# Kernel tuning notes

Hardware: AMD Instinct MI355X
Metric: run time of the kernel (lower is better)

Reference implementation:

```python
import jax, jax.numpy as jnp
import numpy as np

B_, L_ = 32, 4096
D_MODEL, D_STATE, D_CONV, EXPAND, N_LAYERS, HORIZON = 128, 16, 4, 2, 4, 1
D_INNER = EXPAND * D_MODEL
DT_RANK = (D_MODEL + 15) // 16  # ceil(d_model/16) = 8
EPS = 1e-6


def setup_inputs() -> dict:
    key = jax.random.key(0)
    ks = jax.random.split(key, 10)
    s = lambda k, sh, sc: jax.random.normal(k, sh, jnp.float32) * sc
    inp = {}
    inp["x"] = s(ks[0], (B_, L_, 1), 1.0)
    inp["input_proj_w"] = s(ks[1], (D_MODEL, 1), 0.5)
    inp["input_proj_b"] = jnp.zeros((D_MODEL,), jnp.float32)
    inp["in_proj_w"] = s(ks[2], (N_LAYERS, 2 * D_INNER, D_MODEL), D_MODEL ** -0.5)
    inp["conv_w"] = s(ks[3], (N_LAYERS, D_INNER, 1, D_CONV), D_CONV ** -0.5)
    inp["conv_b"] = jnp.zeros((N_LAYERS, D_INNER), jnp.float32)
    inp["x_proj_w"] = s(ks[4], (N_LAYERS, DT_RANK + 2 * D_STATE, D_INNER), D_INNER ** -0.5)
    inp["dt_proj_w"] = s(ks[5], (N_LAYERS, D_INNER, DT_RANK), DT_RANK ** -0.5)
    inp["dt_proj_b"] = jnp.full((N_LAYERS, D_INNER), -4.0, jnp.float32)
    inp["A_log"] = jnp.tile(jnp.log(jnp.arange(1, D_STATE + 1, dtype=jnp.float32))[None, None, :], (N_LAYERS, D_INNER, 1))
    inp["D"] = jnp.ones((N_LAYERS, D_INNER), jnp.float32)
    inp["out_proj_w"] = s(ks[6], (N_LAYERS, D_MODEL, D_INNER), D_INNER ** -0.5)
    inp["norm_w"] = jnp.ones((D_MODEL,), jnp.float32)
    inp["output_proj_w"] = s(ks[7], (HORIZON, D_MODEL), D_MODEL ** -0.5)
    inp["output_proj_b"] = jnp.zeros((HORIZON,), jnp.float32)
    return inp


def _mamba_block(h, in_w, cw, cb, xpw, dtw, dtb, alog, d_skip, ow):
    # h: [B, L, d_model] -> [B, L, d_model]
    xz = jnp.einsum('bld,ed->ble', h, in_w)            # [B, L, 2*d_inner]
    x, z = jnp.split(xz, 2, axis=-1)                   # each [B, L, d_inner]
    # depthwise causal conv over time
    xc = jax.lax.conv_general_dilated(
        x.transpose(0, 2, 1), cw, window_strides=(1,),
        padding=[(D_CONV - 1, 0)], feature_group_count=D_INNER,
        dimension_numbers=('NCH', 'OIH', 'NCH'))      # [B, d_inner, L]
    x = jax.nn.silu(xc.transpose(0, 2, 1) + cb)        # [B, L, d_inner]
    dbl = jnp.einsum('blc,ec->ble', x, xpw)            # [B, L, dt_rank+2*d_state]
    dt, Bm, Cm = jnp.split(dbl, [DT_RANK, DT_RANK + D_STATE], axis=-1)
    dt = jax.nn.softplus(jnp.einsum('blr,cr->blc', dt, dtw) + dtb)  # [B, L, d_inner]
    A = -jnp.exp(alog)                                  # [d_inner, d_state]

    def step(hst, inputs):
        dt_t, B_t, C_t, x_t = inputs                   # [B,c],[B,s],[B,s],[B,c]
        hst = jnp.exp(dt_t[..., None] * A) * hst + (dt_t * x_t)[..., None] * B_t[:, None, :]
        y = jnp.einsum('bcs,bs->bc', hst, C_t)
        return hst, y

    h0 = jnp.zeros((x.shape[0], D_INNER, D_STATE), x.dtype)
    xs = (dt.transpose(1, 0, 2), Bm.transpose(1, 0, 2), Cm.transpose(1, 0, 2), x.transpose(1, 0, 2))
    _, ys = jax.lax.scan(step, h0, xs)                 # [L, B, d_inner]
    y = ys.transpose(1, 0, 2) + d_skip * x             # skip: y += D * x
    y = y * jax.nn.silu(z)                             # gating
    return jnp.einsum('blc,dc->bld', y, ow)            # [B, L, d_model]


def reference(x, input_proj_w, input_proj_b, in_proj_w, conv_w, conv_b, x_proj_w,
              dt_proj_w, dt_proj_b, A_log, D, out_proj_w, norm_w,
              output_proj_w, output_proj_b):
    h = jnp.einsum('blo,do->bld', x, input_proj_w) + input_proj_b  # [B, L, d_model]
    for i in range(N_LAYERS):
        h = h + _mamba_block(h, in_proj_w[i], conv_w[i], conv_b[i], x_proj_w[i],
                             dt_proj_w[i], dt_proj_b[i], A_log[i], D[i], out_proj_w[i])
    rms = jnp.sqrt(jnp.mean(h * h, axis=-1, keepdims=True) + EPS)
    h = norm_w * h / rms
    return h[:, -1, :] @ output_proj_w.T + output_proj_b  # [B, horizon]
```

## Files before the change

### kernel.cpp

```cpp
#include <hip/hip_runtime.h>

#define B_    32
#define L_    4096
#define DM    128
#define DI    256
#define DS_   16
#define RANK  8
#define NL    4
#define M_    (B_*L_)
#define NC    64
#define CL    (L_/NC)

typedef __attribute__((ext_vector_type(8))) short short8;
typedef __attribute__((ext_vector_type(4))) float floatx4;
typedef __attribute__((ext_vector_type(2))) float float2v;

__device__ __forceinline__ float b2f(unsigned short u) {
    return __uint_as_float(((unsigned)u) << 16);
}
__device__ __forceinline__ unsigned short f2b(float f) {
    unsigned u = __float_as_uint(f);
    unsigned r = u + 0x7fffu + ((u >> 16) & 1u);
    return (unsigned short)(r >> 16);
}
__device__ __forceinline__ float fast_sig(float v) {
    return __builtin_amdgcn_rcpf(1.f + __expf(-v));
}

__global__ __launch_bounds__(256) void k_detect(const unsigned short* __restrict__ x,
                                                int* __restrict__ flag) {
    __shared__ int cnt;
    if (threadIdx.x == 0) cnt = 0;
    __syncthreads();
    int ok = 0;
    for (int i = 0; i < 4; ++i) {
        unsigned short u = x[threadIdx.x * 4 + i];
        int e = (u >> 7) & 0xFF;
        if ((u & 0x7FFF) == 0 || (e >= 100 && e <= 150)) ok++;
    }
    atomicAdd(&cnt, ok);
    __syncthreads();
    if (threadIdx.x == 0) *flag = (cnt >= 800) ? 1 : 0;
}

struct CvtSeg { const void* src; float* dst; int n; };
struct CvtPack { CvtSeg seg[11]; };
__global__ __launch_bounds__(256) void k_cvt_params(CvtPack p, const int* __restrict__ flag) {
    int s = blockIdx.y;
    int i = blockIdx.x * 256 + threadIdx.x;
    if (i >= p.seg[s].n) return;
    p.seg[s].dst[i] = (*flag) ? b2f(((const unsigned short*)p.seg[s].src)[i])
                              : ((const float*)p.seg[s].src)[i];
}
__global__ __launch_bounds__(256) void k_cvt16(const void* __restrict__ src,
                                               unsigned short* __restrict__ dst,
                                               int n, const int* __restrict__ flag) {
    int i = blockIdx.x * 256 + threadIdx.x;
    if (i >= n) return;
    if (*flag) dst[i] = ((const unsigned short*)src)[i];
    else       dst[i] = f2b(((const float*)src)[i]);
}
__global__ __launch_bounds__(256) void k_xpw48(const void* __restrict__ src,
                                               unsigned short* __restrict__ dst,
                                               const int* __restrict__ flag) {
    int i = blockIdx.x * 256 + threadIdx.x;
    int col = i & 255, rowl = (i >> 8) % 48, layer = i / (48*256);
    unsigned short v = 0;
    if (rowl < 40) {
        int si = (layer*40 + rowl)*256 + col;
        v = (*flag) ? ((const unsigned short*)src)[si] : f2b(((const float*)src)[si]);
    }
    dst[i] = v;
}

__global__ __launch_bounds__(256) void k_init(const void* __restrict__ xraw,
                                              const int* __restrict__ flag,
                                              const float* __restrict__ ipw,
                                              const float* __restrict__ ipb,
                                              float* __restrict__ h, int base) {
    int idx = blockIdx.x * 256 + threadIdx.x;
    int bl = idx >> 7, d = idx & 127;
    float x = (*flag) ? b2f(((const unsigned short*)xraw)[base + bl])
                      : ((const float*)xraw)[base + bl];
    h[idx] = x * ipw[d] + ipb[d];
}

__global__ __launch_bounds__(256) void k_gemm_in(const float* __restrict__ h,
                                                 const unsigned short* __restrict__ w,
                                                 unsigned short* __restrict__ xb,
                                                 unsigned short* __restrict__ zb) {
    __shared__ unsigned short lA[64][136];
    __shared__ unsigned short lW[256][40];
    int tid = threadIdx.x;
    int lane = tid & 63, wv = tid >> 6;
    int ln = lane & 15, qd = lane >> 4;
    int r0 = blockIdx.x * 64;
    int n0 = blockIdx.y * 256;

    {
        int r = tid >> 2;
        int c0 = (tid & 3) * 32;
        const float4* src = (const float4*)(h + (size_t)(r0 + r) * DM + c0);
        for (int j = 0; j < 8; ++j) {
            float4 v = src[j];
            lA[r][c0 + j*4 + 0] = f2b(v.x);
            lA[r][c0 + j*4 + 1] = f2b(v.y);
            lA[r][c0 + j*4 + 2] = f2b(v.z);
            lA[r][c0 + j*4 + 3] = f2b(v.w);
        }
    }

    floatx4 acc[16];
    for (int i = 0; i < 16; ++i) acc[i] = (floatx4)0.f;

    for (int kc = 0; kc < 4; ++kc) {
        __syncthreads();
        {
            int n = tid;
            const uint4* src = (const uint4*)(w + (size_t)(n0 + n) * DM + kc * 32);
            uint4 a = src[0], b = src[1], c = src[2], d = src[3];
            *(uint4*)&lW[n][0]  = a;
            *(uint4*)&lW[n][8]  = b;
            *(uint4*)&lW[n][16] = c;
            *(uint4*)&lW[n][24] = d;
        }
        __syncthreads();
        short8 af = *(const short8*)&lA[wv*16 + ln][kc*32 + qd*8];
        for (int nt = 0; nt < 16; ++nt) {
            short8 bf = *(const short8*)&lW[nt*16 + ln][qd*8];
            acc[nt] = __builtin_amdgcn_mfma_f32_16x16x32_bf16(af, bf, acc[nt], 0, 0, 0);
        }
    }

    for (int nt = 0; nt < 16; ++nt)
        for (int rg = 0; rg < 4; ++rg) {
            size_t gr = (size_t)(r0 + wv*16 + qd*4 + rg);
            int gc = nt*16 + ln;
            unsigned short v = f2b(acc[nt][rg]);
            if (blockIdx.y == 0) xb[gr*DI + gc] = v;
            else                 zb[gr*DI + gc] = v;
        }
}

__device__ __forceinline__ bool a_is_integer_ladder(const float* A) {
    bool f = true;
    #pragma unroll
    for (int s = 0; s < DS_; ++s)
        f = f && (fabsf(A[s] + (float)(s+1)) < 0.01f * (float)(s+1));
    return f;
}

__device__ __forceinline__ void unpack8(uint4 p, float* f) {
    f[0] = b2f((unsigned short)(p.x & 0xffff)); f[1] = b2f((unsigned short)(p.x >> 16));
    f[2] = b2f((unsigned short)(p.y & 0xffff)); f[3] = b2f((unsigned short)(p.y >> 16));
    f[4] = b2f((unsigned short)(p.z & 0xffff)); f[5] = b2f((unsigned short)(p.z >> 16));
    f[6] = b2f((unsigned short)(p.w & 0xffff)); f[7] = b2f((unsigned short)(p.w >> 16));
}

__global__ __launch_bounds__(256) void k_xprojc(const unsigned short* __restrict__ xb,
                                                const float* __restrict__ cw,
                                                const float* __restrict__ cbp,
                                                const unsigned short* __restrict__ w48,
                                                const float* __restrict__ dtw,
                                                const float* __restrict__ dtb,
                                                const float* __restrict__ alog,
                                                unsigned short* __restrict__ xcg,
                                                unsigned short* __restrict__ dtg,
                                                unsigned short* __restrict__ Bg,
                                                unsigned short* __restrict__ Cg,
                                                float* __restrict__ Pbuf,
                                                float* __restrict__ Hbuf) {
    __shared__ unsigned short lA[64][264];
    __shared__ unsigned short lW[48][40];
    __shared__ float ldbl[64][8];
    __shared__ float lBs[64][DS_];
    int tid = threadIdx.x;
    int lane = tid & 63, wv = tid >> 6;
    int ln = lane & 15, qd = lane >> 4;
    int r0 = blockIdx.x * 64;
    int l0 = r0 & (L_ - 1);
    int bidx = r0 >> 12;
    int kidx = l0 >> 6;

    {
        int c = tid;
        float w0 = cw[c*4+0], w1 = cw[c*4+1], w2 = cw[c*4+2], w3 = cw[c*4+3];
        float bias = cbp[c];
        float x0 = (l0 >= 3) ? b2f(xb[(size_t)(r0-3)*DI + c]) : 0.f;
        float x1 = (l0 >= 2) ? b2f(xb[(size_t)(r0-2)*DI + c]) : 0.f;
        float x2 = (l0 >= 1) ? b2f(xb[(size_t)(r0-1)*DI + c]) : 0.f;
        for (int r = 0; r < 64; ++r) {
            float xcur = b2f(xb[(size_t)(r0+r)*DI + c]);
            float v = w0*x0 + w1*x1 + w2*x2 + w3*xcur + bias;
            float s = v * fast_sig(v);
            unsigned short sb = f2b(s);
            lA[r][c] = sb;
            xcg[(size_t)(r0+r)*DI + c] = sb;
            x0 = x1; x1 = x2; x2 = xcur;
        }
    }

    floatx4 acc[3];
    for (int i = 0; i < 3; ++i) acc[i] = (floatx4)0.f;

    for (int kc = 0; kc < 8; ++kc) {
        __syncthreads();
        if (tid < 192) {
            int n = tid >> 2, q = tid & 3;
            *(uint4*)&lW[n][q*8] = *(const uint4*)(w48 + (size_t)n*DI + kc*32 + q*8);
        }
        __syncthreads();
        short8 af = *(const short8*)&lA[wv*16 + ln][kc*32 + qd*8];
        for (int nt = 0; nt < 3; ++nt) {
            short8 bf = *(const short8*)&lW[nt*16 + ln][qd*8];
            acc[nt] = __builtin_amdgcn_mfma_f32_16x16x32_bf16(af, bf, acc[nt], 0, 0, 0);
        }
    }

    for (int nt = 0; nt < 3; ++nt)
        for (int rg = 0; rg < 4; ++rg) {
            int rloc = wv*16 + qd*4 + rg;
            size_t row = (size_t)(r0 + rloc);
            int n = nt*16 + ln;
            float v = acc[nt][rg];
            if (n < 8)       ldbl[rloc][n] = v;
            else if (n < 24) {
                unsigned short bv = f2b(v);
                Bg[row*DS_ + (n-8)] = bv;
                lBs[rloc][n-8] = b2f(bv);
            }
            else if (n < 40) Cg[row*DS_ + (n-24)] = f2b(v);
        }
    __syncthreads();

    {
        int c = tid;
        float w8[8];
        #pragma unroll
        for (int j = 0; j < 8; ++j) w8[j] = dtw[c*8 + j];
        float bias = dtb[c];
        float A[DS_];
        #pragma unroll
        for (int j = 0; j < 4; ++j) {
            float4 a4 = *(const float4*)(alog + c*DS_ + j*4);
            A[j*4+0] = -__expf(a4.x); A[j*4+1] = -__expf(a4.y);
            A[j*4+2] = -__expf(a4.z); A[j*4+3] = -__expf(a4.w);
        }
        float P[DS_];
        if (a_is_integer_ladder(A)) {
            float2v h2[8];
            #pragma unroll
            for (int j = 0; j < 8; ++j) h2[j] = (float2v)0.f;
            float S = 0.f;
            for (int r = 0; r < 64; ++r) {
                float a = bias;
                #pragma unroll
                for (int j = 0; j < 8; ++j) a += ldbl[r][j] * w8[j];
                float sp = (a > 20.f) ? a : __logf(1.f + __expf(a));
                unsigned short spb = f2b(sp);
                dtg[(size_t)(r0+r)*DI + c] = spb;
                float dtv = b2f(spb);
                float du = dtv * b2f(lA[r][c]);
                float Bl[DS_];
                *(float4*)&Bl[0]  = *(const float4*)&lBs[r][0];
                *(float4*)&Bl[4]  = *(const float4*)&lBs[r][4];
                *(float4*)&Bl[8]  = *(const float4*)&lBs[r][8];
                *(float4*)&Bl[12] = *(const float4*)&lBs[r][12];
                float E = __expf(-dtv);
                float E2 = E * E;
                float2v ep[8];
                ep[0].x = E; ep[0].y = E2;
                float2v E22; E22.x = E2; E22.y = E2;
                #pragma unroll
                for (int j = 1; j < 8; ++j) ep[j] = ep[j-1] * E22;
                float2v du2; du2.x = du; du2.y = du;
                #pragma unroll
                for (int j = 0; j < 8; ++j) {
                    float2v bj; bj.x = Bl[2*j]; bj.y = Bl[2*j+1];
                    h2[j] = ep[j]*h2[j] + du2*bj;
                }
                S += dtv;
            }
            #pragma unroll
            for (int s = 0; s < DS_; ++s) P[s] = __expf(-(float)(s+1) * S);
            float4* pp = (float4*)(Pbuf + (((size_t)bidx*NC + kidx)*DI + c)*DS_);
            float4* ph = (float4*)(Hbuf + (((size_t)bidx*NC + kidx)*DI + c)*DS_);
            #pragma unroll
            for (int j = 0; j < 4; ++j) {
                pp[j] = make_float4(P[j*4+0], P[j*4+1], P[j*4+2], P[j*4+3]);
                ph[j] = make_float4(h2[j*2].x, h2[j*2].y, h2[j*2+1].x, h2[j*2+1].y);
            }
        } else {
            float h[DS_];
            #pragma unroll
            for (int s = 0; s < DS_; ++s) { h[s] = 0.f; P[s] = 1.f; }
            for (int r = 0; r < 64; ++r) {
                float a = bias;
                #pragma unroll
                for (int j = 0; j < 8; ++j) a += ldbl[r][j] * w8[j];
                float sp = (a > 20.f) ? a : __logf(1.f + __expf(a));
                unsigned short spb = f2b(sp);
                dtg[(size_t)(r0+r)*DI + c] = spb;
                float dtv = b2f(spb);
                float du = dtv * b2f(lA[r][c]);
                float Bl[DS_];
                *(float4*)&Bl[0]  = *(const float4*)&lBs[r][0];
                *(float4*)&Bl[4]  = *(const float4*)&lBs[r][4];
                *(float4*)&Bl[8]  = *(const float4*)&lBs[r][8];
                *(float4*)&Bl[12] = *(const float4*)&lBs[r][12];
                #pragma unroll
                for (int s = 0; s < DS_; ++s) {
                    float e = __expf(dtv * A[s]);
                    h[s] = e*h[s] + du*Bl[s];
                    P[s] *= e;
                }
            }
            float4* pp = (float4*)(Pbuf + (((size_t)bidx*NC + kidx)*DI + c)*DS_);
            float4* ph = (float4*)(Hbuf + (((size_t)bidx*NC + kidx)*DI + c)*DS_);
            #pragma unroll
            for (int j = 0; j < 4; ++j) {
                pp[j] = make_float4(P[j*4+0], P[j*4+1], P[j*4+2], P[j*4+3]);
                ph[j] = make_float4(h[j*4+0], h[j*4+1], h[j*4+2], h[j*4+3]);
            }
        }
    }
}

__global__ __launch_bounds__(256) void k_scan2(const float* __restrict__ Pbuf,
                                               float* __restrict__ Hbuf,
                                               int cb) {
    int t = blockIdx.x * 256 + threadIdx.x;
    if (t >= cb * DI * DS_) return;
    int b  = t / (DI * DS_);
    int cs = t % (DI * DS_);
    float H = 0.f;
    for (int k = 0; k < NC; ++k) {
        size_t idx = ((size_t)b * NC + k) * (DI * DS_) + cs;
        float P  = Pbuf[idx];
        float he = Hbuf[idx];
        Hbuf[idx] = H;
        H = P * H + he;
    }
}

__global__ __launch_bounds__(256) void k_scan3g(const unsigned short* __restrict__ dtg,
                                                const unsigned short* __restrict__ xcg,
                                                const unsigned short* __restrict__ Bg,
                                                const unsigned short* __restrict__ Cg,
                                                const float* __restrict__ alog,
                                                const float* __restrict__ Hbuf,
                                                const unsigned short* __restrict__ zb,
                                                const float* __restrict__ Dp,
                                                unsigned short* __restrict__ yg) {
    __shared__ float lB[CL*DS_];
    __shared__ float lC[CL*DS_];
    int c = threadIdx.x;
    int k = blockIdx.x, b = blockIdx.y;
    size_t row0 = (size_t)b * L_ + (size_t)k * CL;
    {
        int t = c & 127;
        const unsigned short* src = (c < 128) ? (Bg + row0*DS_) : (Cg + row0*DS_);
        float* dst = (c < 128) ? lB : lC;
        uint4 p = ((const uint4*)src)[t];
        float f[8]; unpack8(p, f);
        *(float4*)&dst[t*8]     = make_float4(f[0], f[1], f[2], f[3]);
        *(float4*)&dst[t*8 + 4] = make_float4(f[4], f[5], f[6], f[7]);
    }
    float A[DS_];
    #pragma unroll
    for (int j = 0; j < 4; ++j) {
        float4 a4 = *(const float4*)(alog + c*DS_ + j*4);
        A[j*4+0] = -__expf(a4.x); A[j*4+1] = -__expf(a4.y);
        A[j*4+2] = -__expf(a4.z); A[j*4+3] = -__expf(a4.w);
    }
    float Dc = Dp[c];
    __syncthreads();
    const unsigned short* pdt = dtg + row0*DI + c;
    const unsigned short* pxc = xcg + row0*DI + c;
    const unsigned short* pz  = zb  + row0*DI + c;
    unsigned short* py        = yg  + row0*DI + c;
    float dtc = b2f(*pdt), xcc = b2f(*pxc), zc = b2f(*pz);

    if (a_is_integer_ladder(A)) {
        float2v h2[8];
        {
            const float4* ph = (const float4*)(Hbuf + (((size_t)b*NC + k)*DI + c)*DS_);
            #pragma unroll
            for (int j = 0; j < 4; ++j) {
                float4 v = ph[j];
                h2[j*2].x = v.x; h2[j*2].y = v.y;
                h2[j*2+1].x = v.z; h2[j*2+1].y = v.w;
            }
        }
        for (int l = 0; l < CL; ++l) {
            float dtn = b2f(pdt[DI]); float xcn = b2f(pxc[DI]); float zn = b2f(pz[DI]);
            float du = dtc * xcc;
            float Bl[DS_], Cl[DS_];
            *(float4*)&Bl[0]  = *(const float4*)&lB[l*DS_ + 0];
            *(float4*)&Bl[4]  = *(const float4*)&lB[l*DS_ + 4];
            *(float4*)&Bl[8]  = *(const float4*)&lB[l*DS_ + 8];
            *(float4*)&Bl[12] = *(const float4*)&lB[l*DS_ + 12];
            *(float4*)&Cl[0]  = *(const float4*)&lC[l*DS_ + 0];
            *(float4*)&Cl[4]  = *(const float4*)&lC[l*DS_ + 4];
            *(float4*)&Cl[8]  = *(const float4*)&lC[l*DS_ + 8];
            *(float4*)&Cl[12] = *(const float4*)&lC[l*DS_ + 12];
            float E = __expf(-dtc);
            float E2 = E * E;
            float2v ep[8];
            ep[0].x = E; ep[0].y = E2;
            float2v E22; E22.x = E2; E22.y = E2;
            #pragma unroll
            for (int j = 1; j < 8; ++j) ep[j] = ep[j-1] * E22;
            float2v du2; du2.x = du; du2.y = du;
            float2v y2 = (float2v)0.f;
            #pragma unroll
            for (int j = 0; j < 8; ++j) {
                float2v bj; bj.x = Bl[2*j]; bj.y = Bl[2*j+1];
                float2v cj; cj.x = Cl[2*j]; cj.y = Cl[2*j+1];
                h2[j] = ep[j]*h2[j] + du2*bj;
                y2 = y2 + h2[j]*cj;
            }
            float y = y2.x + y2.y;
            *py = f2b((y + Dc*xcc) * (zc * fast_sig(zc)));
            dtc = dtn; xcc = xcn; zc = zn;
            pdt += DI; pxc += DI; pz += DI; py += DI;
        }
    } else {
        float h[DS_];
        {
            const float4* ph = (const float4*)(Hbuf + (((size_t)b*NC + k)*DI + c)*DS_);
            #pragma unroll
            for (int j = 0; j < 4; ++j) {
                float4 v = ph[j];
                h[j*4+0] = v.x; h[j*4+1] = v.y; h[j*4+2] = v.z; h[j*4+3] = v.w;
            }
        }
        for (int l = 0; l < CL; ++l) {
            float dtn = b2f(pdt[DI]); float xcn = b2f(pxc[DI]); float zn = b2f(pz[DI]);
            float du = dtc * xcc;
            float Bl[DS_], Cl[DS_];
            *(float4*)&Bl[0]  = *(const float4*)&lB[l*DS_ + 0];
            *(float4*)&Bl[4]  = *(const float4*)&lB[l*DS_ + 4];
            *(float4*)&Bl[8]  = *(const float4*)&lB[l*DS_ + 8];
            *(float4*)&Bl[12] = *(const float4*)&lB[l*DS_ + 12];
            *(float4*)&Cl[0]  = *(const float4*)&lC[l*DS_ + 0];
            *(float4*)&Cl[4]  = *(const float4*)&lC[l*DS_ + 4];
            *(float4*)&Cl[8]  = *(const float4*)&lC[l*DS_ + 8];
            *(float4*)&Cl[12] = *(const float4*)&lC[l*DS_ + 12];
            float y = 0.f;
            #pragma unroll
            for (int s = 0; s < DS_; ++s) {
                float e = __expf(dtc * A[s]);
                h[s] = e*h[s] + du*Bl[s];
                y += h[s]*Cl[s];
            }
            *py = f2b((y + Dc*xcc) * (zc * fast_sig(zc)));
            dtc = dtn; xcc = xcn; zc = zn;
            pdt += DI; pxc += DI; pz += DI; py += DI;
        }
    }
}

__global__ __launch_bounds__(256) void k_gemm_out(const unsigned short* __restrict__ yg,
                                                  const unsigned short* __restrict__ w,
                                                  float* __restrict__ h) {
    __shared__ unsigned short lA[64][264];
    __shared__ unsigned short lW[128][40];
    int tid = threadIdx.x;
    int lane = tid & 63, wv = tid >> 6;
    int ln = lane & 15, qd = lane >> 4;
    int r0 = blockIdx.x * 64;

    for (int j = 0; j < 8; ++j) {
        int idx = tid + j*256;
        int r = idx >> 5, q = idx & 31;
        *(uint4*)&lA[r][q*8] = *(const uint4*)(yg + (size_t)(r0 + r)*DI + q*8);
    }

    floatx4 acc[8];
    for (int i = 0; i < 8; ++i) acc[i] = (floatx4)0.f;

    for (int kc = 0; kc < 8; ++kc) {
        __syncthreads();
        {
            int n = tid >> 1, half = tid & 1;
            const uint4* src = (const uint4*)(w + (size_t)n*DI + kc*32 + half*16);
            uint4 a = src[0], b4 = src[1];
            *(uint4*)&lW[n][half*16]     = a;
            *(uint4*)&lW[n][half*16 + 8] = b4;
        }
        __syncthreads();
        short8 af = *(const short8*)&lA[wv*16 + ln][kc*32 + qd*8];
        for (int nt = 0; nt < 8; ++nt) {
            short8 bf = *(const short8*)&lW[nt*16 + ln][qd*8];
            acc[nt] = __builtin_amdgcn_mfma_f32_16x16x32_bf16(af, bf, acc[nt], 0, 0, 0);
        }
    }

    for (int nt = 0; nt < 8; ++nt)
        for (int rg = 0; rg < 4; ++rg) {
            size_t gr = (size_t)(r0 + wv*16 + qd*4 + rg);
            int gc = nt*16 + ln;
            h[gr*DM + gc] += acc[nt][rg];
        }
}

__global__ __launch_bounds__(128) void k_head(const float* __restrict__ h,
                                              const float* __restrict__ nw,
                                              const float* __restrict__ opw,
                                              const float* __restrict__ opb,
                                              float* __restrict__ out) {
    __shared__ float red[4];
    int b = blockIdx.x, d = threadIdx.x;
    float hv = h[((size_t)b*L_ + (L_-1))*DM + d];
    float v = hv * hv;
    for (int off = 1; off < 64; off <<= 1) v += __shfl_xor(v, off);
    if ((d & 63) == 0) red[d >> 6] = v;
    __syncthreads();
    float ss = red[0] + red[1];
    float rms = sqrtf(ss * (1.f/DM) + 1e-6f);
    float hn = nw[d] * hv / rms;
    float pv = hn * opw[d];
    for (int off = 1; off < 64; off <<= 1) pv += __shfl_xor(pv, off);
    if ((d & 63) == 0) red[2 + (d >> 6)] = pv;
    __syncthreads();
    if (d == 0) out[b] = red[2] + red[3] + opb[0];
}

extern "C" void kernel_launch(void* const* d_in, const int* in_sizes, int n_in,
                              void* d_out, int out_size, void* d_ws, size_t ws_size,
                              hipStream_t stream) {
    (void)in_sizes; (void)n_in; (void)out_size;
    float* out = (float*)d_out;

    char* wp = (char*)d_ws;
    int* flag = (int*)wp; wp += 16;
    auto allocf = [&](size_t elems) {
        float* p = (float*)wp;
        wp += (elems * 4 + 15) & ~(size_t)15;
        return p;
    };
    auto alloch = [&](size_t elems) {
        unsigned short* p = (unsigned short*)wp;
        wp += (elems * 2 + 15) & ~(size_t)15;
        return p;
    };
    float* c_ipw  = allocf(DM);
    float* c_ipb  = allocf(DM);
    float* c_cw   = allocf((size_t)NL*DI*4);
    float* c_cb   = allocf((size_t)NL*DI);
    float* c_dtw  = allocf((size_t)NL*DI*RANK);
    float* c_dtb  = allocf((size_t)NL*DI);
    float* c_alog = allocf((size_t)NL*DI*DS_);
    float* c_D    = allocf((size_t)NL*DI);
    float* c_nw   = allocf(DM);
    float* c_opw  = allocf(DM);
    float* c_opb  = allocf(1);
    unsigned short* c_inw16 = alloch((size_t)NL*2*DI*DM);
    unsigned short* c_ow16  = alloch((size_t)NL*DM*DI);
    unsigned short* c_xpw48 = alloch((size_t)NL*48*DI);
    wp = (char*)(((size_t)wp + 255) & ~(size_t)255);

    k_detect<<<1, 256, 0, stream>>>((const unsigned short*)d_in[0], flag);

    CvtPack pk;
    pk.seg[0]  = { d_in[1],  c_ipw,  DM };
    pk.seg[1]  = { d_in[2],  c_ipb,  DM };
    pk.seg[2]  = { d_in[4],  c_cw,   NL*DI*4 };
    pk.seg[3]  = { d_in[5],  c_cb,   NL*DI };
    pk.seg[4]  = { d_in[7],  c_dtw,  NL*DI*RANK };
    pk.seg[5]  = { d_in[8],  c_dtb,  NL*DI };
    pk.seg[6]  = { d_in[9],  c_alog, NL*DI*DS_ };
    pk.seg[7]  = { d_in[10], c_D,    NL*DI };
    pk.seg[8]  = { d_in[12], c_nw,   DM };
    pk.seg[9]  = { d_in[13], c_opw,  DM };
    pk.seg[10] = { d_in[14], c_opb,  1 };
    k_cvt_params<<<dim3(64, 11), 256, 0, stream>>>(pk, flag);
    k_cvt16<<<(int)((NL*2*DI*DM + 255)/256), 256, 0, stream>>>(d_in[3],  c_inw16, NL*2*DI*DM, flag);
    k_cvt16<<<(int)((NL*DM*DI   + 255)/256), 256, 0, stream>>>(d_in[11], c_ow16,  NL*DM*DI,   flag);
    k_xpw48<<<NL*48*DI/256, 256, 0, stream>>>(d_in[6], c_xpw48, flag);

    size_t used  = (size_t)(wp - (char*)d_ws);
    size_t avail = (ws_size > used) ? ws_size - used : 0;
    const size_t perB = (size_t)L_ * 2624 + (size_t)2 * NC * DI * DS_ * 4;
    int cb = B_;
    while (cb > 1 && (size_t)cb * perB > avail) cb >>= 1;
    const int Mc = cb * L_;

    float* h            = (float*)wp;          wp += (size_t)Mc*DM*4;
    unsigned short* xb  = (unsigned short*)wp; wp += (size_t)Mc*DI*2;
    unsigned short* zb  = (unsigned short*)wp; wp += (size_t)Mc*DI*2;
    unsigned short* xcg = (unsigned short*)wp; wp += (size_t)Mc*DI*2;
    unsigned short* dty = (unsigned short*)wp; wp += (size_t)Mc*DI*2;
    unsigned short* Bg  = (unsigned short*)wp; wp += (size_t)Mc*DS_*2;
    unsigned short* Cg  = (unsigned short*)wp; wp += (size_t)Mc*DS_*2;
    float* Pbuf         = (float*)wp;          wp += (size_t)cb*NC*DI*DS_*4;
    float* Hbuf         = (float*)wp;          wp += (size_t)cb*NC*DI*DS_*4;

    const int scan2_blocks = (cb * DI * DS_ + 255) / 256;

    for (int b0 = 0; b0 < B_; b0 += cb) {
        k_init<<<Mc*DM/256, 256, 0, stream>>>(d_in[0], flag, c_ipw, c_ipb, h, b0*L_);
        for (int i = 0; i < NL; ++i) {
            k_gemm_in<<<dim3(Mc/64, 2), 256, 0, stream>>>(h, c_inw16 + (size_t)i*2*DI*DM, xb, zb);
            k_xprojc<<<Mc/64, 256, 0, stream>>>(xb, c_cw + i*DI*4, c_cb + i*DI,
                                                c_xpw48 + (size_t)i*48*DI,
                                                c_dtw + i*DI*RANK, c_dtb + i*DI,
                                                c_alog + i*DI*DS_,
                                                xcg, dty, Bg, Cg, Pbuf, Hbuf);
            k_scan2<<<scan2_blocks, 256, 0, stream>>>(Pbuf, Hbuf, cb);
            k_scan3g<<<dim3(NC, cb), 256, 0, stream>>>(dty, xcg, Bg, Cg, c_alog + i*DI*DS_,
                                                       Hbuf, zb, c_D + i*DI, xb);
            k_gemm_out<<<Mc/64, 256, 0, stream>>>(xb, c_ow16 + (size_t)i*DM*DI, h);
        }
        k_head<<<cb, 128, 0, stream>>>(h, c_nw, c_opw, c_opb, out + b0);
    }
}
```

Measured before the change: 1.496 ms.

## Fuse out-proj with next layer's in-proj and store chunk state in bf16

Adds a k_gemm_oi kernel that computes the out-projection, updates the residual h, and then runs the next layer's in-projection from the bf16 copy of h held in LDS. This removes one launch per layer and one re-read of h from global memory. Separately, the per-chunk P and H scan buffers move from fp32 to bf16, halving their traffic across k_xprojc, k_scan2 and k_scan3g. The bf16 state buffers lower precision on the chunk-boundary carry. The fused kernel also reads y from the same xb buffer it later overwrites, which is safe only because each block reads and writes its own rows.

```diff
diff --git a/kernel.cpp b/kernel.cpp
--- a/kernel.cpp
+++ b/kernel.cpp
@@ -156,6 +156,14 @@
     f[4] = b2f((unsigned short)(p.z & 0xffff)); f[5] = b2f((unsigned short)(p.z >> 16));
     f[6] = b2f((unsigned short)(p.w & 0xffff)); f[7] = b2f((unsigned short)(p.w >> 16));
 }
+__device__ __forceinline__ void pack16(const float* f, uint4* o) {
+    unsigned v[8];
+    #pragma unroll
+    for (int j = 0; j < 8; ++j)
+        v[j] = (unsigned)f2b(f[2*j]) | ((unsigned)f2b(f[2*j+1]) << 16);
+    o[0] = make_uint4(v[0], v[1], v[2], v[3]);
+    o[1] = make_uint4(v[4], v[5], v[6], v[7]);
+}
 
 __global__ __launch_bounds__(256) void k_xprojc(const unsigned short* __restrict__ xb,
                                                 const float* __restrict__ cw,
@@ -168,8 +176,8 @@
                                                 unsigned short* __restrict__ dtg,
                                                 unsigned short* __restrict__ Bg,
                                                 unsigned short* __restrict__ Cg,
-                                                float* __restrict__ Pbuf,
-                                                float* __restrict__ Hbuf) {
+                                                unsigned short* __restrict__ Pbuf,
+                                                unsigned short* __restrict__ Hbuf) {
     __shared__ unsigned short lA[64][264];
     __shared__ unsigned short lW[48][40];
     __shared__ float ldbl[64][8];
@@ -246,7 +254,7 @@
             A[j*4+0] = -__expf(a4.x); A[j*4+1] = -__expf(a4.y);
             A[j*4+2] = -__expf(a4.z); A[j*4+3] = -__expf(a4.w);
         }
-        float P[DS_];
+        float P[DS_], hh[DS_];
         if (a_is_integer_ladder(A)) {
             float2v h2[8];
             #pragma unroll
@@ -283,17 +291,11 @@
             }
             #pragma unroll
             for (int s = 0; s < DS_; ++s) P[s] = __expf(-(float)(s+1) * S);
-            float4* pp = (float4*)(Pbuf + (((size_t)bidx*NC + kidx)*DI + c)*DS_);
-            float4* ph = (float4*)(Hbuf + (((size_t)bidx*NC + kidx)*DI + c)*DS_);
             #pragma unroll
-            for (int j = 0; j < 4; ++j) {
-                pp[j] = make_float4(P[j*4+0], P[j*4+1], P[j*4+2], P[j*4+3]);
-                ph[j] = make_float4(h2[j*2].x, h2[j*2].y, h2[j*2+1].x, h2[j*2+1].y);
-            }
+            for (int j = 0; j < 8; ++j) { hh[2*j] = h2[j].x; hh[2*j+1] = h2[j].y; }
         } else {
-            float h[DS_];
             #pragma unroll
-            for (int s = 0; s < DS_; ++s) { h[s] = 0.f; P[s] = 1.f; }
+            for (int s = 0; s < DS_; ++s) { hh[s] = 0.f; P[s] = 1.f; }
             for (int r = 0; r < 64; ++r) {
                 float a = bias;
                 #pragma unroll
@@ -311,23 +313,23 @@
                 #pragma unroll
                 for (int s = 0; s < DS_; ++s) {
                     float e = __expf(dtv * A[s]);
-                    h[s] = e*h[s] + du*Bl[s];
+                    hh[s] = e*hh[s] + du*Bl[s];
                     P[s] *= e;
                 }
             }
-            float4* pp = (float4*)(Pbuf + (((size_t)bidx*NC + kidx)*DI + c)*DS_);
-            float4* ph = (float4*)(Hbuf + (((size_t)bidx*NC + kidx)*DI + c)*DS_);
-            #pragma unroll
-            for (int j = 0; j < 4; ++j) {
-                pp[j] = make_float4(P[j*4+0], P[j*4+1], P[j*4+2], P[j*4+3]);
-                ph[j] = make_float4(h[j*4+0], h[j*4+1], h[j*4+2], h[j*4+3]);
-            }
-        }
-    }
-}
-
-__global__ __launch_bounds__(256) void k_scan2(const float* __restrict__ Pbuf,
-                                               float* __restrict__ Hbuf,
+        }
+        uint4 op[2], oh[2];
+        pack16(P, op);
+        pack16(hh, oh);
+        uint4* pp = (uint4*)(Pbuf + (((size_t)bidx*NC + kidx)*DI + c)*DS_);
+        uint4* ph = (uint4*)(Hbuf + (((size_t)bidx*NC + kidx)*DI + c)*DS_);
+        pp[0] = op[0]; pp[1] = op[1];
+        ph[0] = oh[0]; ph[1] = oh[1];
+    }
+}
+
+__global__ __launch_bounds__(256) void k_scan2(const unsigned short* __restrict__ Pbuf,
+                                               unsigned short* __restrict__ Hbuf,
                                                int cb) {
     int t = blockIdx.x * 256 + threadIdx.x;
     if (t >= cb * DI * DS_) return;
@@ -336,9 +338,9 @@
     float H = 0.f;
     for (int k = 0; k < NC; ++k) {
         size_t idx = ((size_t)b * NC + k) * (DI * DS_) + cs;
-        float P  = Pbuf[idx];
-        float he = Hbuf[idx];
-        Hbuf[idx] = H;
+        float P  = b2f(Pbuf[idx]);
+        float he = b2f(Hbuf[idx]);
+        Hbuf[idx] = f2b(H);
         H = P * H + he;
     }
 }
@@ -348,7 +350,7 @@
                                                 const unsigned short* __restrict__ Bg,
                                                 const unsigned short* __restrict__ Cg,
                                                 const float* __restrict__ alog,
-                                                const float* __restrict__ Hbuf,
+                                                const unsigned short* __restrict__ Hbuf,
                                                 const unsigned short* __restrict__ zb,
                                                 const float* __restrict__ Dp,
                                                 unsigned short* __restrict__ yg) {
@@ -374,6 +376,13 @@
         A[j*4+2] = -__expf(a4.z); A[j*4+3] = -__expf(a4.w);
     }
     float Dc = Dp[c];
+    float h0[DS_];
+    {
+        const uint4* ph = (const uint4*)(Hbuf + (((size_t)b*NC + k)*DI + c)*DS_);
+        uint4 p0 = ph[0], p1 = ph[1];
+        unpack8(p0, &h0[0]);
+        unpack8(p1, &h0[8]);
+    }
     __syncthreads();
     const unsigned short* pdt = dtg + row0*DI + c;
     const unsigned short* pxc = xcg + row0*DI + c;
@@ -383,15 +392,8 @@
 
     if (a_is_integer_ladder(A)) {
         float2v h2[8];
-        {
-            const float4* ph = (const float4*)(Hbuf + (((size_t)b*NC + k)*DI + c)*DS_);
-            #pragma unroll
-            for (int j = 0; j < 4; ++j) {
-                float4 v = ph[j];
-                h2[j*2].x = v.x; h2[j*2].y = v.y;
-                h2[j*2+1].x = v.z; h2[j*2+1].y = v.w;
-            }
-        }
+        #pragma unroll
+        for (int j = 0; j < 8; ++j) { h2[j].x = h0[2*j]; h2[j].y = h0[2*j+1]; }
         for (int l = 0; l < CL; ++l) {
             float dtn = b2f(pdt[DI]); float xcn = b2f(pxc[DI]); float zn = b2f(pz[DI]);
             float du = dtc * xcc;
@@ -427,14 +429,8 @@
         }
     } else {
         float h[DS_];
-        {
-            const float4* ph = (const float4*)(Hbuf + (((size_t)b*NC + k)*DI + c)*DS_);
-            #pragma unroll
-            for (int j = 0; j < 4; ++j) {
-                float4 v = ph[j];
-                h[j*4+0] = v.x; h[j*4+1] = v.y; h[j*4+2] = v.z; h[j*4+3] = v.w;
-            }
-        }
+        #pragma unroll
+        for (int s = 0; s < DS_; ++s) h[s] = h0[s];
         for (int l = 0; l < CL; ++l) {
             float dtn = b2f(pdt[DI]); float xcn = b2f(pxc[DI]); float zn = b2f(pz[DI]);
             float du = dtc * xcc;
@@ -458,6 +454,86 @@
             dtc = dtn; xcc = xcn; zc = zn;
             pdt += DI; pxc += DI; pz += DI; py += DI;
         }
+    }
+}
+
+__global__ __launch_bounds__(256) void k_gemm_oi(const unsigned short* yg,
+                                                 const unsigned short* __restrict__ wo,
+                                                 const unsigned short* __restrict__ wi,
+                                                 float* __restrict__ h,
+                                                 unsigned short* xb,
+                                                 unsigned short* __restrict__ zb) {
+    __shared__ unsigned short lA[64*264];
+    __shared__ unsigned short lW[256*40];
+    int tid = threadIdx.x;
+    int lane = tid & 63, wv = tid >> 6;
+    int ln = lane & 15, qd = lane >> 4;
+    int r0 = blockIdx.x * 64;
+
+    for (int j = 0; j < 8; ++j) {
+        int idx = tid + j*256;
+        int r = idx >> 5, q = idx & 31;
+        *(uint4*)&lA[r*264 + q*8] = *(const uint4*)(yg + (size_t)(r0 + r)*DI + q*8);
+    }
+    floatx4 acc1[8];
+    for (int i = 0; i < 8; ++i) acc1[i] = (floatx4)0.f;
+    for (int kc = 0; kc < 8; ++kc) {
+        __syncthreads();
+        {
+            int n = tid >> 1, half = tid & 1;
+            const uint4* src = (const uint4*)(wo + (size_t)n*DI + kc*32 + half*16);
+            uint4 a = src[0], b4 = src[1];
+            *(uint4*)&lW[n*40 + half*16]     = a;
+            *(uint4*)&lW[n*40 + half*16 + 8] = b4;
+        }
+        __syncthreads();
+        short8 af = *(const short8*)&lA[(wv*16 + ln)*264 + kc*32 + qd*8];
+        for (int nt = 0; nt < 8; ++nt) {
+            short8 bf = *(const short8*)&lW[(nt*16 + ln)*40 + qd*8];
+            acc1[nt] = __builtin_amdgcn_mfma_f32_16x16x32_bf16(af, bf, acc1[nt], 0, 0, 0);
+        }
+    }
+    __syncthreads();
+
+    for (int nt = 0; nt < 8; ++nt)
+        for (int rg = 0; rg < 4; ++rg) {
+            int rloc = wv*16 + qd*4 + rg;
+            size_t gr = (size_t)(r0 + rloc);
+            int gc = nt*16 + ln;
+            float hv = h[gr*DM + gc] + acc1[nt][rg];
+            h[gr*DM + gc] = hv;
+            lA[rloc*136 + gc] = f2b(hv);
+        }
+    __syncthreads();
+
+    for (int n0 = 0; n0 < 2; ++n0) {
+        floatx4 acc2[16];
+        for (int i = 0; i < 16; ++i) acc2[i] = (floatx4)0.f;
+        for (int kc = 0; kc < 4; ++kc) {
+            __syncthreads();
+            {
+                int n = tid;
+                const uint4* src = (const uint4*)(wi + (size_t)(n0*256 + n)*DM + kc*32);
+                uint4 a = src[0], b = src[1], c = src[2], d = src[3];
+                *(uint4*)&lW[n*40 + 0]  = a;
+                *(uint4*)&lW[n*40 + 8]  = b;
+                *(uint4*)&lW[n*40 + 16] = c;
+                *(uint4*)&lW[n*40 + 24] = d;
+            }
+            __syncthreads();
+            short8 af = *(const short8*)&lA[(wv*16 + ln)*136 + kc*32 + qd*8];
+            for (int nt = 0; nt < 16; ++nt) {
+                short8 bf = *(const short8*)&lW[(nt*16 + ln)*40 + qd*8];
+                acc2[nt] = __builtin_amdgcn_mfma_f32_16x16x32_bf16(af, bf, acc2[nt], 0, 0, 0);
+            }
+        }
+        unsigned short* dst = (n0 == 0) ? xb : zb;
+        for (int nt = 0; nt < 16; ++nt)
+            for (int rg = 0; rg < 4; ++rg) {
+                size_t gr = (size_t)(r0 + wv*16 + qd*4 + rg);
+                int gc = nt*16 + ln;
+                dst[gr*DI + gc] = f2b(acc2[nt][rg]);
+            }
     }
 }
 
@@ -582,7 +658,7 @@
 
     size_t used  = (size_t)(wp - (char*)d_ws);
     size_t avail = (ws_size > used) ? ws_size - used : 0;
-    const size_t perB = (size_t)L_ * 2624 + (size_t)2 * NC * DI * DS_ * 4;
+    const size_t perB = (size_t)L_ * 2624 + (size_t)2 * NC * DI * DS_ * 2;
     int cb = B_;
     while (cb > 1 && (size_t)cb * perB > avail) cb >>= 1;
     const int Mc = cb * L_;
@@ -594,15 +670,15 @@
     unsigned short* dty = (unsigned short*)wp; wp += (size_t)Mc*DI*2;
     unsigned short* Bg  = (unsigned short*)wp; wp += (size_t)Mc*DS_*2;
     unsigned short* Cg  = (unsigned short*)wp; wp += (size_t)Mc*DS_*2;
-    float* Pbuf         = (float*)wp;          wp += (size_t)cb*NC*DI*DS_*4;
-    float* Hbuf         = (float*)wp;          wp += (size_t)cb*NC*DI*DS_*4;
+    unsigned short* Pbuf = (unsigned short*)wp; wp += (size_t)cb*NC*DI*DS_*2;
+    unsigned short* Hbuf = (unsigned short*)wp; wp += (size_t)cb*NC*DI*DS_*2;
 
     const int scan2_blocks = (cb * DI * DS_ + 255) / 256;
 
     for (int b0 = 0; b0 < B_; b0 += cb) {
         k_init<<<Mc*DM/256, 256, 0, stream>>>(d_in[0], flag, c_ipw, c_ipb, h, b0*L_);
+        k_gemm_in<<<dim3(Mc/64, 2), 256, 0, stream>>>(h, c_inw16, xb, zb);
         for (int i = 0; i < NL; ++i) {
-            k_gemm_in<<<dim3(Mc/64, 2), 256, 0, stream>>>(h, c_inw16 + (size_t)i*2*DI*DM, xb, zb);
             k_xprojc<<<Mc/64, 256, 0, stream>>>(xb, c_cw + i*DI*4, c_cb + i*DI,
                                                 c_xpw48 + (size_t)i*48*DI,
                                                 c_dtw + i*DI*RANK, c_dtb + i*DI,
@@ -611,7 +687,12 @@
             k_scan2<<<scan2_blocks, 256, 0, stream>>>(Pbuf, Hbuf, cb);
             k_scan3g<<<dim3(NC, cb), 256, 0, stream>>>(dty, xcg, Bg, Cg, c_alog + i*DI*DS_,
                                                        Hbuf, zb, c_D + i*DI, xb);
-            k_gemm_out<<<Mc/64, 256, 0, stream>>>(xb, c_ow16 + (size_t)i*DM*DI, h);
+            if (i < NL-1)
+                k_gemm_oi<<<Mc/64, 256, 0, stream>>>(xb, c_ow16 + (size_t)i*DM*DI,
+                                                     c_inw16 + (size_t)(i+1)*2*DI*DM,
+                                                     h, xb, zb);
+            else
+                k_gemm_out<<<Mc/64, 256, 0, stream>>>(xb, c_ow16 + (size_t)i*DM*DI, h);
         }
         k_head<<<cb, 128, 0, stream>>>(h, c_nw, c_opw, c_opb, out + b0);
     }
```

New measurement: 1.378 ms. 7.9% less time.
